# Kernel tuning notes

Hardware: AMD Instinct MI355X
Metric: run time of the kernel (lower is better)

Reference implementation:

```python
import jax, jax.numpy as jnp
import numpy as np

B, T, S, H = 4, 128, 512, 512
LN_EPS = 1e-5


def setup_inputs() -> dict:
    key = jax.random.key(0)
    ks = jax.random.split(key, 10)
    query = jax.random.normal(ks[0], (B, T, H), dtype=jnp.float32)
    encoder_outputs = jax.random.normal(ks[1], (B, S, H), dtype=jnp.float32)
    src_lengths = jax.random.randint(ks[2], (B,), 1, S + 1, dtype=jnp.int32)
    # Parameters (nn.Linear stores weight as (out, in); we apply x @ W.T)
    W_h = jax.random.normal(ks[3], (H, H), dtype=jnp.float32) / np.sqrt(H)
    W_s = jax.random.normal(ks[4], (H, H), dtype=jnp.float32) / np.sqrt(H)
    v = jax.random.normal(ks[5], (H,), dtype=jnp.float32) * 0.01
    W_out = jax.random.normal(ks[6], (H, 2 * H), dtype=jnp.float32) / np.sqrt(2 * H)
    b_out = jnp.zeros((H,), dtype=jnp.float32)
    gamma = jnp.ones((H,), dtype=jnp.float32)
    beta = jnp.zeros((H,), dtype=jnp.float32)
    return {
        "query": query, "encoder_outputs": encoder_outputs, "src_lengths": src_lengths,
        "W_h": W_h, "W_s": W_s, "v": v, "W_out": W_out, "b_out": b_out,
        "gamma": gamma, "beta": beta,
    }


def reference(query, encoder_outputs, src_lengths, W_h, W_s, v, W_out, b_out, gamma, beta):
    # Project query and encoder states: (b,t,h) and (b,s,h)
    q_proj = jnp.einsum('bth,oh->bto', query, W_s)
    k_proj = jnp.einsum('bsh,oh->bso', encoder_outputs, W_h)
    # Additive score: tanh over broadcast-add, then dot with v -> (b,t,s)
    score = jnp.einsum('btsh,h->bts', jnp.tanh(q_proj[:, :, None, :] + k_proj[:, None, :, :]), v)
    # Mask padded source positions (src_idx >= length)
    pad = jnp.arange(S)[None, :] >= src_lengths[:, None]          # (b,s)
    score = jnp.where(pad[:, None, :], -jnp.inf, score)
    attn = jax.nn.softmax(score, axis=-1)                          # (b,t,s)
    context = jnp.einsum('bts,bsh->bth', attn, encoder_outputs)    # (b,t,h)
    cq = jnp.concatenate([context, query], axis=-1)                # (b,t,2h)
    out = jnp.tanh(jnp.einsum('btk,ok->bto', cq, W_out) + b_out)
    # LayerNorm over last dim
    mu = jnp.mean(out, axis=-1, keepdims=True)
    var = jnp.mean(jnp.square(out - mu), axis=-1, keepdims=True)
    return (out - mu) / jnp.sqrt(var + LN_EPS) * gamma + beta
```

## Files before the change

### kernel.cpp

```cpp
#include <hip/hip_runtime.h>
#include <hip/hip_bf16.h>
#include <math.h>

#define B 4
#define T 128
#define S 512
#define H 512
#define QK_SCALE 2.8853900817779268f

#if defined(__has_builtin)
#if __has_builtin(__builtin_amdgcn_exp2f)
#define EXP2F(x) __builtin_amdgcn_exp2f(x)
#else
#define EXP2F(x) __expf((x) * 0.6931471805599453f)
#endif
#else
#define EXP2F(x) __expf((x) * 0.6931471805599453f)
#endif

typedef __attribute__((ext_vector_type(8))) short bf16x8;
typedef __attribute__((ext_vector_type(4))) float f32x4;

__device__ __forceinline__ short f2b(float x) {
    unsigned int u = __float_as_uint(x);
    u += 0x7fffu + ((u >> 16) & 1u);
    return (short)(u >> 16);
}
__device__ __forceinline__ float fast_tanh(float x) {
    float e = __expf(2.0f * x);
    float r = __builtin_amdgcn_rcpf(e + 1.0f);
    return 1.0f - 2.0f * r;
}

__global__ __launch_bounds__(256) void cvt_all(
    const float* __restrict__ q, const float* __restrict__ Ws,
    const float* __restrict__ Wh, const float* __restrict__ Wo,
    const float* __restrict__ enc,
    short* __restrict__ qb, short* __restrict__ wsb, short* __restrict__ whb,
    short* __restrict__ wob, short* __restrict__ eb) {
    size_t i = ((size_t)blockIdx.x * 256 + threadIdx.x) * 8;
    const float* src; short* dst; size_t off;
    if (i < 262144)        { src = q;   dst = qb;  off = i; }
    else if (i < 524288)   { src = Ws;  dst = wsb; off = i - 262144; }
    else if (i < 786432)   { src = Wh;  dst = whb; off = i - 524288; }
    else if (i < 1310720)  { src = Wo;  dst = wob; off = i - 786432; }
    else                   { src = enc; dst = eb;  off = i - 1310720; }
    float4 a = *(const float4*)(src + off);
    float4 b = *(const float4*)(src + off + 4);
    ushort4 o0 = make_ushort4((unsigned short)f2b(a.x), (unsigned short)f2b(a.y),
                              (unsigned short)f2b(a.z), (unsigned short)f2b(a.w));
    ushort4 o1 = make_ushort4((unsigned short)f2b(b.x), (unsigned short)f2b(b.y),
                              (unsigned short)f2b(b.z), (unsigned short)f2b(b.w));
    *(ushort4*)(dst + off) = o0;
    *(ushort4*)(dst + off + 4) = o1;
}

__global__ __launch_bounds__(64) void proj_mega(
    const short* __restrict__ qb, const short* __restrict__ eb,
    const short* __restrict__ wsb, const short* __restrict__ whb,
    const short* __restrict__ wob, const int* __restrict__ slen,
    float* __restrict__ qe, float* __restrict__ keT,
    short* __restrict__ ewt, float* __restrict__ qw) {
    const int job = blockIdx.x;
    const int lane = threadIdx.x;
    const int r = lane & 15, kb = lane >> 4;
    const short* A; int lda;
    const short* W; int ldw;
    int epi;
    float* Cf = nullptr; short* Cb = nullptr; int ldc;
    int bT = 0, m0T = 0, n0T = 0;
    if (job < 256) {
        const int m0 = (job >> 4) * 32, n0 = (job & 15) * 32;
        A = qb + (size_t)m0 * H; lda = H;
        W = wsb + (size_t)n0 * H; ldw = H;
        Cf = qe + (size_t)m0 * H + n0; ldc = H; epi = 0;
    } else if (job < 1280) {
        const int j = job - 256;
        const int m0 = (j >> 4) * 32, n0 = (j & 15) * 32;
        if ((m0 & 511) >= slen[m0 >> 9]) return;
        A = eb + (size_t)m0 * H; lda = H;
        W = whb + (size_t)n0 * H; ldw = H;
        epi = 3; bT = m0 >> 9; m0T = m0 & 511; n0T = n0;
    } else if (job < 2304) {
        const int j = job - 1280;
        const int b = j >> 8;
        const int m0 = ((j >> 4) & 15) * 32;
        const int n0 = (j & 15) * 32;
        if (n0 >= slen[b]) return;
        A = wob + (size_t)m0 * (2 * H); lda = 2 * H;
        W = eb + ((size_t)b * S + n0) * H; ldw = H;
        Cb = ewt + (size_t)b * H * S + (size_t)m0 * S + n0; ldc = S; epi = 1;
    } else {
        const int j = job - 2304;
        const int m0 = (j >> 4) * 32, n0 = (j & 15) * 32;
        A = qb + (size_t)m0 * H; lda = H;
        W = wob + (size_t)n0 * (2 * H) + H; ldw = 2 * H;
        Cf = qw + (size_t)m0 * H + n0; ldc = H; epi = 2;
    }
    const short* a0p = A + (size_t)r * lda + kb * 8;
    const short* a1p = a0p + (size_t)16 * lda;
    const short* b0p = W + (size_t)r * ldw + kb * 8;
    const short* b1p = b0p + (size_t)16 * ldw;
    f32x4 acc00 = {0,0,0,0}, acc01 = {0,0,0,0}, acc10 = {0,0,0,0}, acc11 = {0,0,0,0};
#pragma unroll 4
    for (int k = 0; k < H; k += 32) {
        bf16x8 a0 = *(const bf16x8*)(a0p + k);
        bf16x8 a1 = *(const bf16x8*)(a1p + k);
        bf16x8 b0 = *(const bf16x8*)(b0p + k);
        bf16x8 b1 = *(const bf16x8*)(b1p + k);
        acc00 = __builtin_amdgcn_mfma_f32_16x16x32_bf16(a0, b0, acc00, 0, 0, 0);
        acc01 = __builtin_amdgcn_mfma_f32_16x16x32_bf16(a0, b1, acc01, 0, 0, 0);
        acc10 = __builtin_amdgcn_mfma_f32_16x16x32_bf16(a1, b0, acc10, 0, 0, 0);
        acc11 = __builtin_amdgcn_mfma_f32_16x16x32_bf16(a1, b1, acc11, 0, 0, 0);
    }
    const int cr = kb * 4, cc = r;
    if (epi == 3) {
        float* base = keT + ((size_t)bT * H + n0T + cc) * S + m0T + cr;
        float4 w00 = make_float4(EXP2F(acc00[0] * QK_SCALE), EXP2F(acc00[1] * QK_SCALE),
                                 EXP2F(acc00[2] * QK_SCALE), EXP2F(acc00[3] * QK_SCALE));
        float4 w01 = make_float4(EXP2F(acc01[0] * QK_SCALE), EXP2F(acc01[1] * QK_SCALE),
                                 EXP2F(acc01[2] * QK_SCALE), EXP2F(acc01[3] * QK_SCALE));
        float4 w10 = make_float4(EXP2F(acc10[0] * QK_SCALE), EXP2F(acc10[1] * QK_SCALE),
                                 EXP2F(acc10[2] * QK_SCALE), EXP2F(acc10[3] * QK_SCALE));
        float4 w11 = make_float4(EXP2F(acc11[0] * QK_SCALE), EXP2F(acc11[1] * QK_SCALE),
                                 EXP2F(acc11[2] * QK_SCALE), EXP2F(acc11[3] * QK_SCALE));
        *(float4*)base              = w00;
        *(float4*)(base + 16 * S)   = w01;
        *(float4*)(base + 16)       = w10;
        *(float4*)(base + 16 * S + 16) = w11;
    } else if (epi == 0) {
#pragma unroll
        for (int g = 0; g < 4; ++g) {
            Cf[(size_t)(cr + g) * ldc + cc]           = EXP2F(acc00[g] * QK_SCALE);
            Cf[(size_t)(cr + g) * ldc + 16 + cc]      = EXP2F(acc01[g] * QK_SCALE);
            Cf[(size_t)(16 + cr + g) * ldc + cc]      = EXP2F(acc10[g] * QK_SCALE);
            Cf[(size_t)(16 + cr + g) * ldc + 16 + cc] = EXP2F(acc11[g] * QK_SCALE);
        }
    } else if (epi == 1) {
#pragma unroll
        for (int g = 0; g < 4; ++g) {
            Cb[(size_t)(cr + g) * ldc + cc]           = f2b(acc00[g]);
            Cb[(size_t)(cr + g) * ldc + 16 + cc]      = f2b(acc01[g]);
            Cb[(size_t)(16 + cr + g) * ldc + cc]      = f2b(acc10[g]);
            Cb[(size_t)(16 + cr + g) * ldc + 16 + cc] = f2b(acc11[g]);
        }
    } else {
#pragma unroll
        for (int g = 0; g < 4; ++g) {
            Cf[(size_t)(cr + g) * ldc + cc]           = acc00[g];
            Cf[(size_t)(cr + g) * ldc + 16 + cc]      = acc01[g];
            Cf[(size_t)(16 + cr + g) * ldc + cc]      = acc10[g];
            Cf[(size_t)(16 + cr + g) * ldc + 16 + cc] = acc11[g];
        }
    }
}

__global__ __launch_bounds__(64) void score_v7(
    const float* __restrict__ qe, const float* __restrict__ keT,
    const float* __restrict__ v, const int* __restrict__ slen,
    float* __restrict__ scoreh) {
    const int qt = blockIdx.z & 3;
    const int b = blockIdx.z >> 2;
    const int L = slen[b];
    const int sbase = blockIdx.x * 64;
    if (sbase >= L) return;
    const int t0 = blockIdx.y * 4;
    const int hbase = qt * 128;
    __shared__ __align__(16) float qs[4][132];
    __shared__ __align__(16) float vsh[128];
    const int lane = threadIdx.x;
    {
        const int tr = lane >> 4, c = (lane & 15) * 8;
        const float* qsrc = qe + (size_t)(b * T + t0 + tr) * H + hbase + c;
        *(float4*)&qs[tr][c]     = *(const float4*)qsrc;
        *(float4*)&qs[tr][c + 4] = *(const float4*)(qsrc + 4);
        if (lane < 32) {
            float4 vv = *(const float4*)&v[hbase + lane * 4];
            *(float4*)&vsh[lane * 4] =
                make_float4(-2.f * vv.x, -2.f * vv.y, -2.f * vv.z, -2.f * vv.w);
        }
    }
    __syncthreads();
    const float* kcol = keT + ((size_t)b * H + hbase) * S + sbase + lane;
    float acc0 = 0.f, acc1 = 0.f, acc2 = 0.f, acc3 = 0.f;
#pragma unroll 8
    for (int h = 0; h < 128; ++h) {
        float kv = kcol[(size_t)h * S];
        float vh = vsh[h];
        float q0 = qs[0][h], q1 = qs[1][h], q2 = qs[2][h], q3 = qs[3][h];
        acc0 = fmaf(vh, __builtin_amdgcn_rcpf(fmaf(q0, kv, 1.f)), acc0);
        acc1 = fmaf(vh, __builtin_amdgcn_rcpf(fmaf(q1, kv, 1.f)), acc1);
        acc2 = fmaf(vh, __builtin_amdgcn_rcpf(fmaf(q2, kv, 1.f)), acc2);
        acc3 = fmaf(vh, __builtin_amdgcn_rcpf(fmaf(q3, kv, 1.f)), acc3);
    }
    const size_t obase = ((size_t)qt * (B * T) + b * T + t0) * S + sbase + lane;
    scoreh[obase]         = acc0;
    scoreh[obase + S]     = acc1;
    scoreh[obase + 2 * S] = acc2;
    scoreh[obase + 3 * S] = acc3;
}

__global__ __launch_bounds__(256) void combine_k(
    const float* __restrict__ scoreh, const int* __restrict__ slen,
    short* __restrict__ U, float* __restrict__ Z) {
    const int row = blockIdx.x * 4 + (threadIdx.x >> 6);
    const int lane = threadIdx.x & 63;
    const int L = slen[row >> 7];
    const size_t sl = (size_t)(B * T) * S;
    const float* p = scoreh + (size_t)row * S + lane * 8;
    float e[8];
    float sm = 0.f;
#pragma unroll
    for (int j = 0; j < 2; ++j) {
        float4 q0 = *(const float4*)(p + j * 4);
        float4 q1 = *(const float4*)(p + sl + j * 4);
        float4 q2 = *(const float4*)(p + 2 * sl + j * 4);
        float4 q3 = *(const float4*)(p + 3 * sl + j * 4);
        e[j * 4 + 0] = __expf(q0.x + q1.x + q2.x + q3.x);
        e[j * 4 + 1] = __expf(q0.y + q1.y + q2.y + q3.y);
        e[j * 4 + 2] = __expf(q0.z + q1.z + q2.z + q3.z);
        e[j * 4 + 3] = __expf(q0.w + q1.w + q2.w + q3.w);
    }
    const int cbase = lane * 8;
#pragma unroll
    for (int j = 0; j < 8; ++j) {
        if (cbase + j >= L) e[j] = 0.f;
        sm += e[j];
    }
#pragma unroll
    for (int off = 1; off < 64; off <<= 1) sm += __shfl_xor(sm, off);
    if (lane == 0) Z[row] = sm;
    short* o = U + (size_t)row * S + cbase;
    ushort4 u0 = make_ushort4((unsigned short)f2b(e[0]), (unsigned short)f2b(e[1]),
                              (unsigned short)f2b(e[2]), (unsigned short)f2b(e[3]));
    ushort4 u1 = make_ushort4((unsigned short)f2b(e[4]), (unsigned short)f2b(e[5]),
                              (unsigned short)f2b(e[6]), (unsigned short)f2b(e[7]));
    *(ushort4*)o = u0;
    *(ushort4*)(o + 4) = u1;
}

__global__ __launch_bounds__(64) void mfma_out2(
    const short* __restrict__ U, const short* __restrict__ ewt,
    const float* __restrict__ qw, const float* __restrict__ Z,
    const int* __restrict__ slen, const float* __restrict__ bias,
    float* __restrict__ pre) {
    const int lane = threadIdx.x;
    const int r = lane & 15, kb = lane >> 4;
    const int m0 = blockIdx.y * 32;
    const int n0 = blockIdx.x * 32;
    const int b = m0 >> 7;
    const int L = slen[b];
    const int Keff = min(S, (L + 31) & ~31);
    const short* A = U + (size_t)m0 * S;
    const short* Bp = ewt + (size_t)b * H * S;
    const short* a0p = A + (size_t)r * S + kb * 8;
    const short* a1p = a0p + 16 * S;
    const short* b0p = Bp + (size_t)(n0 + r) * S + kb * 8;
    const short* b1p = b0p + 16 * S;
    f32x4 acc00 = {0,0,0,0}, acc01 = {0,0,0,0}, acc10 = {0,0,0,0}, acc11 = {0,0,0,0};
#pragma unroll 2
    for (int k = 0; k < Keff; k += 32) {
        bf16x8 a0 = *(const bf16x8*)(a0p + k);
        bf16x8 a1 = *(const bf16x8*)(a1p + k);
        bf16x8 b0 = *(const bf16x8*)(b0p + k);
        bf16x8 b1 = *(const bf16x8*)(b1p + k);
        acc00 = __builtin_amdgcn_mfma_f32_16x16x32_bf16(a0, b0, acc00, 0, 0, 0);
        acc01 = __builtin_amdgcn_mfma_f32_16x16x32_bf16(a0, b1, acc01, 0, 0, 0);
        acc10 = __builtin_amdgcn_mfma_f32_16x16x32_bf16(a1, b0, acc10, 0, 0, 0);
        acc11 = __builtin_amdgcn_mfma_f32_16x16x32_bf16(a1, b1, acc11, 0, 0, 0);
    }
    const int cr = kb * 4, cc = r;
    float bn0 = bias[n0 + cc], bn1 = bias[n0 + 16 + cc];
#pragma unroll
    for (int g = 0; g < 4; ++g) {
        const int gr0 = m0 + cr + g;
        const int gr1 = gr0 + 16;
        float iz0 = __builtin_amdgcn_rcpf(Z[gr0]);
        float iz1 = __builtin_amdgcn_rcpf(Z[gr1]);
        size_t row0 = (size_t)gr0 * H;
        size_t row1 = (size_t)gr1 * H;
        pre[row0 + n0 + cc]      = fast_tanh(fmaf(acc00[g], iz0, qw[row0 + n0 + cc]) + bn0);
        pre[row0 + n0 + 16 + cc] = fast_tanh(fmaf(acc01[g], iz0, qw[row0 + n0 + 16 + cc]) + bn1);
        pre[row1 + n0 + cc]      = fast_tanh(fmaf(acc10[g], iz1, qw[row1 + n0 + cc]) + bn0);
        pre[row1 + n0 + 16 + cc] = fast_tanh(fmaf(acc11[g], iz1, qw[row1 + n0 + 16 + cc]) + bn1);
    }
}

__global__ __launch_bounds__(256) void ln_out(
    const float* __restrict__ X, const float* __restrict__ gamma,
    const float* __restrict__ beta, float* __restrict__ out) {
    __shared__ float red[8];
    const int r = blockIdx.x;
    const int tid = threadIdx.x;
    const int lane = tid & 63, wv = tid >> 6;
    const float* x = X + (size_t)r * H;
    float x0 = x[tid], x1 = x[tid + 256];
    float s = x0 + x1;
#pragma unroll
    for (int off = 32; off > 0; off >>= 1) s += __shfl_down(s, off);
    if (lane == 0) red[wv] = s;
    __syncthreads();
    float mu = (red[0] + red[1] + red[2] + red[3]) * (1.0f / H);
    float d0 = x0 - mu, d1 = x1 - mu;
    float vsum = d0 * d0 + d1 * d1;
#pragma unroll
    for (int off = 32; off > 0; off >>= 1) vsum += __shfl_down(vsum, off);
    if (lane == 0) red[4 + wv] = vsum;
    __syncthreads();
    float var = (red[4] + red[5] + red[6] + red[7]) * (1.0f / H);
    float inv = rsqrtf(var + 1e-5f);
    out[(size_t)r * H + tid] = d0 * inv * gamma[tid] + beta[tid];
    out[(size_t)r * H + tid + 256] = d1 * inv * gamma[tid + 256] + beta[tid + 256];
}

extern "C" void kernel_launch(void* const* d_in, const int* in_sizes, int n_in,
                              void* d_out, int out_size, void* d_ws, size_t ws_size,
                              hipStream_t stream) {
    const float* query = (const float*)d_in[0];
    const float* enc   = (const float*)d_in[1];
    const int*   slen  = (const int*)d_in[2];
    const float* W_h   = (const float*)d_in[3];
    const float* W_s   = (const float*)d_in[4];
    const float* v     = (const float*)d_in[5];
    const float* W_out = (const float*)d_in[6];
    const float* b_out = (const float*)d_in[7];
    const float* gamma = (const float*)d_in[8];
    const float* beta  = (const float*)d_in[9];
    float* out = (float*)d_out;

    char* base = (char*)d_ws;
    short* qb     = (short*)(base + 0x000000);
    short* wsb    = (short*)(base + 0x080000);
    short* whb    = (short*)(base + 0x100000);
    short* wob    = (short*)(base + 0x180000);
    short* eb     = (short*)(base + 0x280000);
    float* qe     = (float*)(base + 0x480000);
    float* keT    = (float*)(base + 0x580000);
    float* scoreh = (float*)(base + 0x980000);
    short* U      = (short*)(base + 0xD80000);
    short* ewt    = (short*)(base + 0xE00000);
    float* qw     = (float*)(base + 0x1000000);
    float* Z      = (float*)(base + 0x1100000);
    float* pre    = (float*)(base + 0x1101000);

    cvt_all<<<dim3(1152), dim3(256), 0, stream>>>(query, W_s, W_h, W_out, enc,
                                                  qb, wsb, whb, wob, eb);
    proj_mega<<<dim3(2560), dim3(64), 0, stream>>>(qb, eb, wsb, whb, wob, slen,
                                                   qe, keT, ewt, qw);
    score_v7<<<dim3(8, 32, 16), dim3(64), 0, stream>>>(qe, keT, v, slen, scoreh);
    combine_k<<<dim3(128), dim3(256), 0, stream>>>(scoreh, slen, U, Z);
    mfma_out2<<<dim3(16, 16), dim3(64), 0, stream>>>(U, ewt, qw, Z, slen, b_out, pre);
    ln_out<<<dim3(B * T), dim3(256), 0, stream>>>(pre, gamma, beta, out);
}
```

Before: 62.51 us.

## Fuse bf16 conversion into projection GEMM and softmax exp into score kernel

Removes the separate fp32-to-bf16 conversion kernel: the projection GEMM now loads fp32 operands and converts them to bf16 in registers. Also merges the score and combine kernels. Each 128-thread block covers the full hidden dimension with two waves, reduces their partial sums through shared memory, applies exp and masking, writes bf16 U, and stores per-chunk partial row sums. The output GEMM then sums those partials to get the normaliser. This cuts two launches and the scoreh round trip through memory, at the cost of doubled fp32 operand traffic in the GEMM and fewer, heavier score blocks.

```diff
diff --git a/kernel.cpp b/kernel.cpp
--- a/kernel.cpp
+++ b/kernel.cpp
@@ -31,55 +31,40 @@
     float r = __builtin_amdgcn_rcpf(e + 1.0f);
     return 1.0f - 2.0f * r;
 }
-
-__global__ __launch_bounds__(256) void cvt_all(
-    const float* __restrict__ q, const float* __restrict__ Ws,
-    const float* __restrict__ Wh, const float* __restrict__ Wo,
-    const float* __restrict__ enc,
-    short* __restrict__ qb, short* __restrict__ wsb, short* __restrict__ whb,
-    short* __restrict__ wob, short* __restrict__ eb) {
-    size_t i = ((size_t)blockIdx.x * 256 + threadIdx.x) * 8;
-    const float* src; short* dst; size_t off;
-    if (i < 262144)        { src = q;   dst = qb;  off = i; }
-    else if (i < 524288)   { src = Ws;  dst = wsb; off = i - 262144; }
-    else if (i < 786432)   { src = Wh;  dst = whb; off = i - 524288; }
-    else if (i < 1310720)  { src = Wo;  dst = wob; off = i - 786432; }
-    else                   { src = enc; dst = eb;  off = i - 1310720; }
-    float4 a = *(const float4*)(src + off);
-    float4 b = *(const float4*)(src + off + 4);
-    ushort4 o0 = make_ushort4((unsigned short)f2b(a.x), (unsigned short)f2b(a.y),
-                              (unsigned short)f2b(a.z), (unsigned short)f2b(a.w));
-    ushort4 o1 = make_ushort4((unsigned short)f2b(b.x), (unsigned short)f2b(b.y),
-                              (unsigned short)f2b(b.z), (unsigned short)f2b(b.w));
-    *(ushort4*)(dst + off) = o0;
-    *(ushort4*)(dst + off + 4) = o1;
+__device__ __forceinline__ bf16x8 ld_cvt8(const float* p) {
+    float4 a = *(const float4*)p;
+    float4 c = *(const float4*)(p + 4);
+    bf16x8 r;
+    r[0] = f2b(a.x); r[1] = f2b(a.y); r[2] = f2b(a.z); r[3] = f2b(a.w);
+    r[4] = f2b(c.x); r[5] = f2b(c.y); r[6] = f2b(c.z); r[7] = f2b(c.w);
+    return r;
 }
 
 __global__ __launch_bounds__(64) void proj_mega(
-    const short* __restrict__ qb, const short* __restrict__ eb,
-    const short* __restrict__ wsb, const short* __restrict__ whb,
-    const short* __restrict__ wob, const int* __restrict__ slen,
+    const float* __restrict__ query, const float* __restrict__ enc,
+    const float* __restrict__ Ws, const float* __restrict__ Wh,
+    const float* __restrict__ Wo, const int* __restrict__ slen,
     float* __restrict__ qe, float* __restrict__ keT,
     short* __restrict__ ewt, float* __restrict__ qw) {
     const int job = blockIdx.x;
     const int lane = threadIdx.x;
     const int r = lane & 15, kb = lane >> 4;
-    const short* A; int lda;
-    const short* W; int ldw;
+    const float* A; int lda;
+    const float* W; int ldw;
     int epi;
-    float* Cf = nullptr; short* Cb = nullptr; int ldc;
+    float* Cf = nullptr; short* Cb = nullptr; int ldc = 0;
     int bT = 0, m0T = 0, n0T = 0;
     if (job < 256) {
         const int m0 = (job >> 4) * 32, n0 = (job & 15) * 32;
-        A = qb + (size_t)m0 * H; lda = H;
-        W = wsb + (size_t)n0 * H; ldw = H;
+        A = query + (size_t)m0 * H; lda = H;
+        W = Ws + (size_t)n0 * H; ldw = H;
         Cf = qe + (size_t)m0 * H + n0; ldc = H; epi = 0;
     } else if (job < 1280) {
         const int j = job - 256;
         const int m0 = (j >> 4) * 32, n0 = (j & 15) * 32;
         if ((m0 & 511) >= slen[m0 >> 9]) return;
-        A = eb + (size_t)m0 * H; lda = H;
-        W = whb + (size_t)n0 * H; ldw = H;
+        A = enc + (size_t)m0 * H; lda = H;
+        W = Wh + (size_t)n0 * H; ldw = H;
         epi = 3; bT = m0 >> 9; m0T = m0 & 511; n0T = n0;
     } else if (job < 2304) {
         const int j = job - 1280;
@@ -87,27 +72,25 @@
         const int m0 = ((j >> 4) & 15) * 32;
         const int n0 = (j & 15) * 32;
         if (n0 >= slen[b]) return;
-        A = wob + (size_t)m0 * (2 * H); lda = 2 * H;
-        W = eb + ((size_t)b * S + n0) * H; ldw = H;
+        A = Wo + (size_t)m0 * (2 * H); lda = 2 * H;
+        W = enc + ((size_t)b * S + n0) * H; ldw = H;
         Cb = ewt + (size_t)b * H * S + (size_t)m0 * S + n0; ldc = S; epi = 1;
     } else {
         const int j = job - 2304;
         const int m0 = (j >> 4) * 32, n0 = (j & 15) * 32;
-        A = qb + (size_t)m0 * H; lda = H;
-        W = wob + (size_t)n0 * (2 * H) + H; ldw = 2 * H;
+        A = query + (size_t)m0 * H; lda = H;
+        W = Wo + (size_t)n0 * (2 * H) + H; ldw = 2 * H;
         Cf = qw + (size_t)m0 * H + n0; ldc = H; epi = 2;
     }
-    const short* a0p = A + (size_t)r * lda + kb * 8;
-    const short* a1p = a0p + (size_t)16 * lda;
-    const short* b0p = W + (size_t)r * ldw + kb * 8;
-    const short* b1p = b0p + (size_t)16 * ldw;
+    const float* a0p = A + (size_t)r * lda + kb * 8;
+    const float* a1p = a0p + (size_t)16 * lda;
+    const float* b0p = W + (size_t)r * ldw + kb * 8;
+    const float* b1p = b0p + (size_t)16 * ldw;
     f32x4 acc00 = {0,0,0,0}, acc01 = {0,0,0,0}, acc10 = {0,0,0,0}, acc11 = {0,0,0,0};
 #pragma unroll 4
     for (int k = 0; k < H; k += 32) {
-        bf16x8 a0 = *(const bf16x8*)(a0p + k);
-        bf16x8 a1 = *(const bf16x8*)(a1p + k);
-        bf16x8 b0 = *(const bf16x8*)(b0p + k);
-        bf16x8 b1 = *(const bf16x8*)(b1p + k);
+        bf16x8 a0 = ld_cvt8(a0p + k), a1 = ld_cvt8(a1p + k);
+        bf16x8 b0 = ld_cvt8(b0p + k), b1 = ld_cvt8(b1p + k);
         acc00 = __builtin_amdgcn_mfma_f32_16x16x32_bf16(a0, b0, acc00, 0, 0, 0);
         acc01 = __builtin_amdgcn_mfma_f32_16x16x32_bf16(a0, b1, acc01, 0, 0, 0);
         acc10 = __builtin_amdgcn_mfma_f32_16x16x32_bf16(a1, b0, acc10, 0, 0, 0);
@@ -124,9 +107,9 @@
                                  EXP2F(acc10[2] * QK_SCALE), EXP2F(acc10[3] * QK_SCALE));
         float4 w11 = make_float4(EXP2F(acc11[0] * QK_SCALE), EXP2F(acc11[1] * QK_SCALE),
                                  EXP2F(acc11[2] * QK_SCALE), EXP2F(acc11[3] * QK_SCALE));
-        *(float4*)base              = w00;
-        *(float4*)(base + 16 * S)   = w01;
-        *(float4*)(base + 16)       = w10;
+        *(float4*)base                 = w00;
+        *(float4*)(base + 16 * S)      = w01;
+        *(float4*)(base + 16)          = w10;
         *(float4*)(base + 16 * S + 16) = w11;
     } else if (epi == 0) {
 #pragma unroll
@@ -155,93 +138,67 @@
     }
 }
 
-__global__ __launch_bounds__(64) void score_v7(
+__global__ __launch_bounds__(128) void score_full(
     const float* __restrict__ qe, const float* __restrict__ keT,
     const float* __restrict__ v, const int* __restrict__ slen,
-    float* __restrict__ scoreh) {
-    const int qt = blockIdx.z & 3;
-    const int b = blockIdx.z >> 2;
+    short* __restrict__ U, float* __restrict__ Zp) {
+    const int chunk = blockIdx.x;
+    const int b = blockIdx.z;
     const int L = slen[b];
-    const int sbase = blockIdx.x * 64;
+    const int sbase = chunk * 64;
     if (sbase >= L) return;
     const int t0 = blockIdx.y * 4;
-    const int hbase = qt * 128;
-    __shared__ __align__(16) float qs[4][132];
-    __shared__ __align__(16) float vsh[128];
-    const int lane = threadIdx.x;
+    const int wv = threadIdx.x >> 6, lane = threadIdx.x & 63;
+    const int hbase = wv * 256;
+    __shared__ __align__(16) float qs[2][4][260];
+    __shared__ __align__(16) float vsh[2][256];
+    __shared__ __align__(16) float psum[2][4][64];
     {
-        const int tr = lane >> 4, c = (lane & 15) * 8;
+        const int tr = lane >> 4, c = (lane & 15) * 16;
         const float* qsrc = qe + (size_t)(b * T + t0 + tr) * H + hbase + c;
-        *(float4*)&qs[tr][c]     = *(const float4*)qsrc;
-        *(float4*)&qs[tr][c + 4] = *(const float4*)(qsrc + 4);
-        if (lane < 32) {
-            float4 vv = *(const float4*)&v[hbase + lane * 4];
-            *(float4*)&vsh[lane * 4] =
-                make_float4(-2.f * vv.x, -2.f * vv.y, -2.f * vv.z, -2.f * vv.w);
-        }
+#pragma unroll
+        for (int j = 0; j < 4; ++j)
+            *(float4*)&qs[wv][tr][c + j * 4] = *(const float4*)(qsrc + j * 4);
+        float4 vv = *(const float4*)&v[hbase + lane * 4];
+        *(float4*)&vsh[wv][lane * 4] =
+            make_float4(-2.f * vv.x, -2.f * vv.y, -2.f * vv.z, -2.f * vv.w);
     }
     __syncthreads();
     const float* kcol = keT + ((size_t)b * H + hbase) * S + sbase + lane;
     float acc0 = 0.f, acc1 = 0.f, acc2 = 0.f, acc3 = 0.f;
 #pragma unroll 8
-    for (int h = 0; h < 128; ++h) {
+    for (int h = 0; h < 256; ++h) {
         float kv = kcol[(size_t)h * S];
-        float vh = vsh[h];
-        float q0 = qs[0][h], q1 = qs[1][h], q2 = qs[2][h], q3 = qs[3][h];
+        float vh = vsh[wv][h];
+        float q0 = qs[wv][0][h], q1 = qs[wv][1][h], q2 = qs[wv][2][h], q3 = qs[wv][3][h];
         acc0 = fmaf(vh, __builtin_amdgcn_rcpf(fmaf(q0, kv, 1.f)), acc0);
         acc1 = fmaf(vh, __builtin_amdgcn_rcpf(fmaf(q1, kv, 1.f)), acc1);
         acc2 = fmaf(vh, __builtin_amdgcn_rcpf(fmaf(q2, kv, 1.f)), acc2);
         acc3 = fmaf(vh, __builtin_amdgcn_rcpf(fmaf(q3, kv, 1.f)), acc3);
     }
-    const size_t obase = ((size_t)qt * (B * T) + b * T + t0) * S + sbase + lane;
-    scoreh[obase]         = acc0;
-    scoreh[obase + S]     = acc1;
-    scoreh[obase + 2 * S] = acc2;
-    scoreh[obase + 3 * S] = acc3;
-}
-
-__global__ __launch_bounds__(256) void combine_k(
-    const float* __restrict__ scoreh, const int* __restrict__ slen,
-    short* __restrict__ U, float* __restrict__ Z) {
-    const int row = blockIdx.x * 4 + (threadIdx.x >> 6);
-    const int lane = threadIdx.x & 63;
-    const int L = slen[row >> 7];
-    const size_t sl = (size_t)(B * T) * S;
-    const float* p = scoreh + (size_t)row * S + lane * 8;
-    float e[8];
-    float sm = 0.f;
-#pragma unroll
-    for (int j = 0; j < 2; ++j) {
-        float4 q0 = *(const float4*)(p + j * 4);
-        float4 q1 = *(const float4*)(p + sl + j * 4);
-        float4 q2 = *(const float4*)(p + 2 * sl + j * 4);
-        float4 q3 = *(const float4*)(p + 3 * sl + j * 4);
-        e[j * 4 + 0] = __expf(q0.x + q1.x + q2.x + q3.x);
-        e[j * 4 + 1] = __expf(q0.y + q1.y + q2.y + q3.y);
-        e[j * 4 + 2] = __expf(q0.z + q1.z + q2.z + q3.z);
-        e[j * 4 + 3] = __expf(q0.w + q1.w + q2.w + q3.w);
-    }
-    const int cbase = lane * 8;
-#pragma unroll
-    for (int j = 0; j < 8; ++j) {
-        if (cbase + j >= L) e[j] = 0.f;
-        sm += e[j];
-    }
-#pragma unroll
-    for (int off = 1; off < 64; off <<= 1) sm += __shfl_xor(sm, off);
-    if (lane == 0) Z[row] = sm;
-    short* o = U + (size_t)row * S + cbase;
-    ushort4 u0 = make_ushort4((unsigned short)f2b(e[0]), (unsigned short)f2b(e[1]),
-                              (unsigned short)f2b(e[2]), (unsigned short)f2b(e[3]));
-    ushort4 u1 = make_ushort4((unsigned short)f2b(e[4]), (unsigned short)f2b(e[5]),
-                              (unsigned short)f2b(e[6]), (unsigned short)f2b(e[7]));
-    *(ushort4*)o = u0;
-    *(ushort4*)(o + 4) = u1;
+    psum[wv][0][lane] = acc0;
+    psum[wv][1][lane] = acc1;
+    psum[wv][2][lane] = acc2;
+    psum[wv][3][lane] = acc3;
+    __syncthreads();
+#pragma unroll
+    for (int rr = 0; rr < 2; ++rr) {
+        const int t = wv * 2 + rr;
+        const int row = b * T + t0 + t;
+        float x = psum[0][t][lane] + psum[1][t][lane];
+        float e = __expf(x);
+        if (sbase + lane >= L) e = 0.f;
+        U[(size_t)row * S + sbase + lane] = f2b(e);
+        float z = e;
+#pragma unroll
+        for (int off = 1; off < 64; off <<= 1) z += __shfl_xor(z, off);
+        if (lane == 0) Zp[(size_t)chunk * (B * T) + row] = z;
+    }
 }
 
 __global__ __launch_bounds__(64) void mfma_out2(
     const short* __restrict__ U, const short* __restrict__ ewt,
-    const float* __restrict__ qw, const float* __restrict__ Z,
+    const float* __restrict__ qw, const float* __restrict__ Zp,
     const int* __restrict__ slen, const float* __restrict__ bias,
     float* __restrict__ pre) {
     const int lane = threadIdx.x;
@@ -251,6 +208,11 @@
     const int b = m0 >> 7;
     const int L = slen[b];
     const int Keff = min(S, (L + 31) & ~31);
+    const int cmax = (L + 63) >> 6;
+    float z = 0.f;
+    for (int c = 0; c < cmax; ++c)
+        z += Zp[(size_t)c * (B * T) + m0 + (lane & 31)];
+    const float iz_r = __builtin_amdgcn_rcpf(z);
     const short* A = U + (size_t)m0 * S;
     const short* Bp = ewt + (size_t)b * H * S;
     const short* a0p = A + (size_t)r * S + kb * 8;
@@ -275,8 +237,8 @@
     for (int g = 0; g < 4; ++g) {
         const int gr0 = m0 + cr + g;
         const int gr1 = gr0 + 16;
-        float iz0 = __builtin_amdgcn_rcpf(Z[gr0]);
-        float iz1 = __builtin_amdgcn_rcpf(Z[gr1]);
+        float iz0 = __shfl(iz_r, cr + g);
+        float iz1 = __shfl(iz_r, 16 + cr + g);
         size_t row0 = (size_t)gr0 * H;
         size_t row1 = (size_t)gr1 * H;
         pre[row0 + n0 + cc]      = fast_tanh(fmaf(acc00[g], iz0, qw[row0 + n0 + cc]) + bn0);
@@ -329,26 +291,17 @@
     float* out = (float*)d_out;
 
     char* base = (char*)d_ws;
-    short* qb     = (short*)(base + 0x000000);
-    short* wsb    = (short*)(base + 0x080000);
-    short* whb    = (short*)(base + 0x100000);
-    short* wob    = (short*)(base + 0x180000);
-    short* eb     = (short*)(base + 0x280000);
-    float* qe     = (float*)(base + 0x480000);
-    float* keT    = (float*)(base + 0x580000);
-    float* scoreh = (float*)(base + 0x980000);
-    short* U      = (short*)(base + 0xD80000);
-    short* ewt    = (short*)(base + 0xE00000);
-    float* qw     = (float*)(base + 0x1000000);
-    float* Z      = (float*)(base + 0x1100000);
-    float* pre    = (float*)(base + 0x1101000);
-
-    cvt_all<<<dim3(1152), dim3(256), 0, stream>>>(query, W_s, W_h, W_out, enc,
-                                                  qb, wsb, whb, wob, eb);
-    proj_mega<<<dim3(2560), dim3(64), 0, stream>>>(qb, eb, wsb, whb, wob, slen,
-                                                   qe, keT, ewt, qw);
-    score_v7<<<dim3(8, 32, 16), dim3(64), 0, stream>>>(qe, keT, v, slen, scoreh);
-    combine_k<<<dim3(128), dim3(256), 0, stream>>>(scoreh, slen, U, Z);
-    mfma_out2<<<dim3(16, 16), dim3(64), 0, stream>>>(U, ewt, qw, Z, slen, b_out, pre);
+    float* qe   = (float*)(base + 0x000000);
+    float* keT  = (float*)(base + 0x100000);
+    short* U    = (short*)(base + 0x500000);
+    short* ewt  = (short*)(base + 0x580000);
+    float* qw   = (float*)(base + 0x780000);
+    float* Zp   = (float*)(base + 0x880000);
+    float* pre  = (float*)(base + 0x884000);
+
+    proj_mega<<<dim3(2560), dim3(64), 0, stream>>>(query, enc, W_s, W_h, W_out,
+                                                   slen, qe, keT, ewt, qw);
+    score_full<<<dim3(8, 32, 4), dim3(128), 0, stream>>>(qe, keT, v, slen, U, Zp);
+    mfma_out2<<<dim3(16, 16), dim3(64), 0, stream>>>(U, ewt, qw, Zp, slen, b_out, pre);
     ln_out<<<dim3(B * T), dim3(256), 0, stream>>>(pre, gamma, beta, out);
 }
```

New measurement: 80.90 us. 29.4% more time.
